# Optimization experiments

Measured on AMD Instinct MI355X. Metric: run time of the kernel, lower is better.

The kernel has to match this reference:

```python
import jax, jax.numpy as jnp
import numpy as np

N_HEAD = 16
N_FEAT = 1024
D_K = N_FEAT // N_HEAD


def setup_inputs() -> dict:
    key = jax.random.key(0)
    ks = jax.random.split(key, 12)
    B, T, F = 4, 2048, N_FEAT
    s = 1.0 / np.sqrt(F)
    return {
        "query": jax.random.normal(ks[0], (B, T, F), dtype=jnp.float32),
        "key": jax.random.normal(ks[1], (B, T, F), dtype=jnp.float32),
        "value": jax.random.normal(ks[2], (B, T, F), dtype=jnp.float32),
        "mask": jnp.ones((B, 1, T), dtype=jnp.int32),
        "Wq": jax.random.normal(ks[3], (F, F), dtype=jnp.float32) * s,
        "bq": jax.random.normal(ks[4], (F,), dtype=jnp.float32) * 0.01,
        "Wk": jax.random.normal(ks[5], (F, F), dtype=jnp.float32) * s,
        "bk": jax.random.normal(ks[6], (F,), dtype=jnp.float32) * 0.01,
        "Wv": jax.random.normal(ks[7], (F, F), dtype=jnp.float32) * s,
        "bv": jax.random.normal(ks[8], (F,), dtype=jnp.float32) * 0.01,
        "Wo": jax.random.normal(ks[9], (F, F), dtype=jnp.float32) * s,
        "bo": jax.random.normal(ks[10], (F,), dtype=jnp.float32) * 0.01,
    }


def reference(query, key, value, mask, Wq, bq, Wk, bk, Wv, bv, Wo, bo):
    B, Tq, F = query.shape
    Tk = key.shape[1]
    h, dk = N_HEAD, D_K
    # torch nn.Linear: y = x @ W.T + b ; then view [B,T,h,dk] and transpose to [B,h,T,dk]
    q = (query @ Wq.T + bq).reshape(B, Tq, h, dk).transpose(0, 2, 1, 3)
    k = (key @ Wk.T + bk).reshape(B, Tk, h, dk).transpose(0, 2, 1, 3)
    v = (value @ Wv.T + bv).reshape(B, Tk, h, dk).transpose(0, 2, 1, 3)
    scale = 1.0 / np.sqrt(dk).astype(np.float32)
    scores = jnp.einsum("bhqd,bhkd->bhqk", q, k) * scale  # [B,h,Tq,Tk]
    # mask [B,1,Tk] -> unsqueeze(1) -> [B,1,1,Tk], True where mask == 0 (padded)
    pad = (mask[:, None, :, :] == 0)
    min_value = jnp.finfo(scores.dtype).min
    scores = jnp.where(pad, min_value, scores)
    atten = jax.nn.softmax(scores, axis=-1)
    atten = jnp.where(pad, 0.0, atten)
    # dropout_rate = 0.0 (eval): identity
    x = jnp.einsum("bhqk,bhkd->bhqd", atten, v)  # [B,h,Tq,dk]
    x = x.transpose(0, 2, 1, 3).reshape(B, Tq, h * dk)
    return x @ Wo.T + bo
```

## Files before the change

### kernel.cpp

```cpp
#include <hip/hip_runtime.h>
#include <hip/hip_bf16.h>


typedef unsigned short u16;
typedef unsigned long long u64;
typedef __attribute__((ext_vector_type(8))) short short8;
typedef __attribute__((ext_vector_type(4))) float f32x4;
typedef __attribute__((ext_vector_type(16))) float f32x16;
typedef __attribute__((ext_vector_type(4))) unsigned int u32x4;

#define GLOAD16(g, l) __builtin_amdgcn_global_load_lds( \
    (const __attribute__((address_space(1))) unsigned int*)(g), \
    (__attribute__((address_space(3))) unsigned int*)(l), 16, 0, 0)

__device__ __forceinline__ u16 f2bf(float x) {
  unsigned int u = __float_as_uint(x);
  return (u16)((u + 0x7fffu + ((u >> 16) & 1u)) >> 16);
}

__device__ __forceinline__ float fexp2(float x) {
#if __has_builtin(__builtin_amdgcn_exp2f)
  return __builtin_amdgcn_exp2f(x);
#else
  return exp2f(x);
#endif
}

__device__ __forceinline__ unsigned cvtpk(float lo, float hi) {
  unsigned r;
  asm("v_cvt_pk_bf16_f32 %0, %1, %2" : "=v"(r) : "v"(lo), "v"(hi));
  return r;
}

struct CvtArgs {
  const float* src[4];
  u16* dst[4];
};

__global__ __launch_bounds__(256) void cvt_multi(CvtArgs a, int shift) {
  const int id = blockIdx.x * 256 + threadIdx.x;
  const int seg = id >> shift;
  const int off = id & ((1 << shift) - 1);
  float4 v = ((const float4*)a.src[seg])[off];
  ushort4 o;
  o.x = f2bf(v.x); o.y = f2bf(v.y); o.z = f2bf(v.z); o.w = f2bf(v.w);
  ((ushort4*)a.dst[seg])[off] = o;
}

template <int EPI, int AF32>
__global__ __launch_bounds__(256) void gemm_bt(const void* __restrict__ Ap,
                                               const u16* __restrict__ Bw,
                                               const float* __restrict__ bias,
                                               void* __restrict__ Cout,
                                               float scale) {
  __shared__ __align__(16) char As[16384];
  __shared__ __align__(16) char Bs[16384];
  const int t = threadIdx.x;
  const int lane = t & 63;
  const int w = t >> 6;
  const int wm = w >> 1, wn = w & 1;
  const int l15 = lane & 15, l4 = lane >> 4;

  const int bid = blockIdx.x;
  const int swz = (bid & 7) * 64 + (bid >> 3);
  const int brow = swz >> 3;
  const int bcol = swz & 7;

  f32x4 acc[4][4] = {};

  const int srow = t >> 3;
  const int sbyte = (t & 7) * 16;
  const int arj = t >> 4;
  const int acol = t & 15;

  for (int kt = 0; kt < 16; ++kt) {
    const int k0 = kt * 64;
    __syncthreads();
    if constexpr (AF32) {
      const float* Ag = (const float*)Ap;
      float4 areg[8];
#pragma unroll
      for (int j = 0; j < 8; ++j)
        areg[j] = *(const float4*)(Ag + (size_t)(brow * 128 + j * 16 + arj) * 1024 +
                                   k0 + acol * 4);
#pragma unroll
      for (int i = 0; i < 4; ++i) {
        const int r = i * 32 + srow;
        const int sb = sbyte ^ ((r & 7) << 4);
        GLOAD16((const char*)(Bw + (size_t)(bcol * 128 + r) * 1024 + k0) + sb,
                Bs + i * 4096 + t * 16);
      }
#pragma unroll
      for (int j = 0; j < 8; ++j) {
        const int r = j * 16 + arj;
        uint2 pk = make_uint2(cvtpk(areg[j].x, areg[j].y), cvtpk(areg[j].z, areg[j].w));
        *(uint2*)(As + r * 128 + ((acol * 8) ^ ((r & 7) << 4))) = pk;
      }
    } else {
      const u16* Ag = (const u16*)Ap;
#pragma unroll
      for (int i = 0; i < 4; ++i) {
        const int r = i * 32 + srow;
        const int sb = sbyte ^ ((r & 7) << 4);
        GLOAD16((const char*)(Ag + (size_t)(brow * 128 + r) * 1024 + k0) + sb,
                As + i * 4096 + t * 16);
        GLOAD16((const char*)(Bw + (size_t)(bcol * 128 + r) * 1024 + k0) + sb,
                Bs + i * 4096 + t * 16);
      }
    }
    __syncthreads();
#pragma unroll
    for (int kf = 0; kf < 2; ++kf) {
      short8 af[4], bfv[4];
#pragma unroll
      for (int mi = 0; mi < 4; ++mi) {
        const int r = wm * 64 + mi * 16 + l15;
        af[mi] = *(const short8*)(As + r * 128 + ((kf * 64 + l4 * 16) ^ ((r & 7) << 4)));
      }
#pragma unroll
      for (int ni = 0; ni < 4; ++ni) {
        const int r = wn * 64 + ni * 16 + l15;
        bfv[ni] = *(const short8*)(Bs + r * 128 + ((kf * 64 + l4 * 16) ^ ((r & 7) << 4)));
      }
#pragma unroll
      for (int mi = 0; mi < 4; ++mi)
#pragma unroll
        for (int ni = 0; ni < 4; ++ni)
          acc[mi][ni] = __builtin_amdgcn_mfma_f32_16x16x32_bf16(
              af[mi], bfv[ni], acc[mi][ni], 0, 0, 0);
    }
  }

#pragma unroll
  for (int ni = 0; ni < 4; ++ni) {
    const int n = bcol * 128 + wn * 64 + ni * 16 + l15;
    const float bn = bias[n];
#pragma unroll
    for (int mi = 0; mi < 4; ++mi) {
      const int mb = brow * 128 + wm * 64 + mi * 16 + l4 * 4;
#pragma unroll
      for (int r = 0; r < 4; ++r) {
        const float v = acc[mi][ni][r] + bn;
        const int m = mb + r;
        const int b_ = m >> 11, tok = m & 2047, h_ = n >> 6, d = n & 63;
        if (EPI == 0) {
          ((u16*)Cout)[(((size_t)(b_ * 16 + h_) * 2048 + tok) << 6) + d] = f2bf(v * scale);
        } else if (EPI == 2) {
          ((u16*)Cout)[(((size_t)(b_ * 16 + h_) * 64 + d) << 11) + tok] = f2bf(v);
        } else {
          ((float*)Cout)[(size_t)m * 1024 + n] = v;
        }
      }
    }
  }
}

__global__ __launch_bounds__(256, 2) void attn_fwd10(const u16* __restrict__ Q,
                                                     const u16* __restrict__ Kp,
                                                     const u16* __restrict__ Vt,
                                                     const int* __restrict__ mask,
                                                     u16* __restrict__ ctx) {
  __shared__ u16 Ks[2][64 * 64];
  __shared__ u16 Vs[2][64 * 64];

  const int t = threadIdx.x, lane = t & 63, w = t >> 6;
  const int q31 = lane & 31, hi = lane >> 5;

  const int bid = blockIdx.x;
  const int swz = (bid & 7) * 64 + (bid >> 3);
  const int bh = swz >> 3;
  const int b_ = bh >> 4, h_ = bh & 15;
  const int q0 = (swz & 7) * 256 + w * 64;
  const size_t headO = (size_t)bh * 131072;

  short8 qfA[4], qfB[4];
  {
    const u16* qrowA = Q + headO + (size_t)(q0 + q31) * 64 + hi * 8;
    const u16* qrowB = qrowA + 32 * 64;
#pragma unroll
    for (int ds = 0; ds < 4; ++ds) {
      qfA[ds] = *(const short8*)(qrowA + ds * 16);
      qfB[ds] = *(const short8*)(qrowB + ds * 16);
    }
  }

  const int srow = t >> 3;
  const int sbyte = (t & 7) * 16;

#define STAGE_KV(bufi, kb)                                                      \
  {                                                                             \
    _Pragma("unroll") for (int i = 0; i < 2; ++i) {                             \
      const int r = i * 32 + srow;                                              \
      const int sb = sbyte ^ ((r & 7) << 4);                                    \
      GLOAD16((const char*)(Kp + headO + (size_t)((kb) + r) * 64) + sb,         \
              &Ks[bufi][(i * 4096 + t * 16) >> 1]);                             \
      GLOAD16((const char*)(Vt + headO + (size_t)r * 2048 + (kb)) + sb,         \
              &Vs[bufi][(i * 4096 + t * 16) >> 1]);                             \
    }                                                                           \
  }

#define SOFTMAX(sA, sB, hh)                                                     \
  {                                                                             \
    if (bits == ~0ull) {                                                        \
      _Pragma("unroll") for (int r = 0; r < 16; ++r) {                          \
        sA[r] = fexp2(sA[r]); sB[r] = fexp2(sB[r]);                             \
      }                                                                         \
    } else {                                                                    \
      _Pragma("unroll") for (int r = 0; r < 16; ++r) {                          \
        const int k0 = (hh) * 32 + (r & 3) + 8 * (r >> 2) + 4 * hi;             \
        const bool on = (bits >> k0) & 1;                                       \
        sA[r] = on ? fexp2(sA[r]) : 0.f;                                        \
        sB[r] = on ? fexp2(sB[r]) : 0.f;                                        \
      }                                                                         \
    }                                                                           \
    float a0 = 0.f, a1 = 0.f, b0 = 0.f, b1 = 0.f;                               \
    _Pragma("unroll") for (int r = 0; r < 16; r += 2) {                         \
      a0 += sA[r]; a1 += sA[r + 1];                                             \
      b0 += sB[r]; b1 += sB[r + 1];                                             \
    }                                                                           \
    lA += a0 + a1;                                                              \
    lB += b0 + b1;                                                              \
  }

#define PACK(sv, pfa, pfb)                                                      \
  {                                                                             \
    const unsigned w0 = cvtpk(sv[0], sv[1]),   w1 = cvtpk(sv[2], sv[3]);        \
    const unsigned w2 = cvtpk(sv[4], sv[5]),   w3 = cvtpk(sv[6], sv[7]);        \
    const unsigned w4 = cvtpk(sv[8], sv[9]),   w5 = cvtpk(sv[10], sv[11]);      \
    const unsigned w6 = cvtpk(sv[12], sv[13]), w7 = cvtpk(sv[14], sv[15]);      \
    const unsigned x0 = (unsigned)__shfl_xor((int)(hi ? w0 : w2), 32);          \
    const unsigned x1 = (unsigned)__shfl_xor((int)(hi ? w1 : w3), 32);          \
    const unsigned y0 = (unsigned)__shfl_xor((int)(hi ? w4 : w6), 32);          \
    const unsigned y1 = (unsigned)__shfl_xor((int)(hi ? w5 : w7), 32);          \
    u32x4 fa = hi ? (u32x4){x0, x1, w2, w3} : (u32x4){w0, w1, x0, x1};          \
    u32x4 fb = hi ? (u32x4){y0, y1, w6, w7} : (u32x4){w4, w5, y0, y1};          \
    pfa = __builtin_bit_cast(short8, fa);                                       \
    pfb = __builtin_bit_cast(short8, fb);                                       \
  }

#define PV(hh, pA0, pA1, pB0, pB1)                                              \
  {                                                                             \
    const int rb0 = q31 * 128, rb1 = (32 + q31) * 128;                          \
    const int c0 = ((hh) * 64 + kcol) ^ rswz;                                   \
    const int c1 = ((hh) * 64 + 32 + kcol) ^ rswz;                              \
    short8 va;                                                                  \
    va = *(const short8*)&Vs[buf][(rb0 + c0) >> 1];                             \
    oA0 = __builtin_amdgcn_mfma_f32_32x32x16_bf16(va, pA0, oA0, 0, 0, 0);       \
    oB0 = __builtin_amdgcn_mfma_f32_32x32x16_bf16(va, pB0, oB0, 0, 0, 0);       \
    va = *(const short8*)&Vs[buf][(rb0 + c1) >> 1];                             \
    oA0 = __builtin_amdgcn_mfma_f32_32x32x16_bf16(va, pA1, oA0, 0, 0, 0);       \
    oB0 = __builtin_amdgcn_mfma_f32_32x32x16_bf16(va, pB1, oB0, 0, 0, 0);       \
    va = *(const short8*)&Vs[buf][(rb1 + c0) >> 1];                             \
    oA1 = __builtin_amdgcn_mfma_f32_32x32x16_bf16(va, pA0, oA1, 0, 0, 0);       \
    oB1 = __builtin_amdgcn_mfma_f32_32x32x16_bf16(va, pB0, oB1, 0, 0, 0);       \
    va = *(const short8*)&Vs[buf][(rb1 + c1) >> 1];                             \
    oA1 = __builtin_amdgcn_mfma_f32_32x32x16_bf16(va, pA1, oA1, 0, 0, 0);       \
    oB1 = __builtin_amdgcn_mfma_f32_32x32x16_bf16(va, pB1, oB1, 0, 0, 0);       \
  }

  f32x16 oA0 = {}, oA1 = {}, oB0 = {}, oB1 = {};
  float lA = 0.f, lB = 0.f;
  const int kcol = hi * 16;
  const int rswz = (q31 & 7) << 4;

  STAGE_KV(0, 0);
  int mk = mask[b_ * 2048 + lane];
  __syncthreads();

  int buf = 0;
  for (int kt = 0; kt < 32; ++kt) {
    const int kb = kt * 64;
    if (kt + 1 < 32) STAGE_KV(buf ^ 1, kb + 64);
    const int mk_next = (kt + 1 < 32) ? mask[b_ * 2048 + kb + 64 + lane] : 0;
    const u64 bits = __ballot(mk != 0);

    f32x16 sA0 = {}, sB0 = {}, sA1 = {}, sB1 = {};
    __builtin_amdgcn_s_setprio(1);
#pragma unroll
    for (int ds = 0; ds < 4; ++ds) {
      const int cb = (ds * 32 + kcol) ^ rswz;
      short8 ka0 = *(const short8*)&Ks[buf][(q31 * 128 + cb) >> 1];
      short8 ka1 = *(const short8*)&Ks[buf][((32 + q31) * 128 + cb) >> 1];
      sA0 = __builtin_amdgcn_mfma_f32_32x32x16_bf16(ka0, qfA[ds], sA0, 0, 0, 0);
      sB0 = __builtin_amdgcn_mfma_f32_32x32x16_bf16(ka0, qfB[ds], sB0, 0, 0, 0);
      sA1 = __builtin_amdgcn_mfma_f32_32x32x16_bf16(ka1, qfA[ds], sA1, 0, 0, 0);
      sB1 = __builtin_amdgcn_mfma_f32_32x32x16_bf16(ka1, qfB[ds], sB1, 0, 0, 0);
    }
    __builtin_amdgcn_s_setprio(0);

    SOFTMAX(sA0, sB0, 0);
    short8 pA0, pA1, pB0, pB1;
    PACK(sA0, pA0, pA1);
    PACK(sB0, pB0, pB1);

    __builtin_amdgcn_s_setprio(1);
    PV(0, pA0, pA1, pB0, pB1);
    __builtin_amdgcn_s_setprio(0);

    SOFTMAX(sA1, sB1, 1);
    PACK(sA1, pA0, pA1);
    PACK(sB1, pB0, pB1);

    __builtin_amdgcn_s_setprio(1);
    PV(1, pA0, pA1, pB0, pB1);
    __builtin_amdgcn_s_setprio(0);

    mk = mk_next;
    __syncthreads();
    buf ^= 1;
  }
#undef STAGE_KV
#undef SOFTMAX
#undef PV

  lA += __shfl_xor(lA, 32);
  lB += __shfl_xor(lB, 32);
  const float invA = lA > 0.f ? 1.f / lA : 0.f;
  const float invB = lB > 0.f ? 1.f / lB : 0.f;
  const int tokA = q0 + q31;
  u16* crowA = ctx + ((size_t)b_ * 2048 + tokA) * 1024 + h_ * 64 + 4 * hi;
  u16* crowB = crowA + 32 * 1024;
#pragma unroll
  for (int g = 0; g < 4; ++g) {
    unsigned u0, u1;
    u0 = cvtpk(oA0[4 * g + 0] * invA, oA0[4 * g + 1] * invA);
    u1 = cvtpk(oA0[4 * g + 2] * invA, oA0[4 * g + 3] * invA);
    *(uint2*)(crowA + 8 * g) = make_uint2(u0, u1);
    u0 = cvtpk(oA1[4 * g + 0] * invA, oA1[4 * g + 1] * invA);
    u1 = cvtpk(oA1[4 * g + 2] * invA, oA1[4 * g + 3] * invA);
    *(uint2*)(crowA + 32 + 8 * g) = make_uint2(u0, u1);
    u0 = cvtpk(oB0[4 * g + 0] * invB, oB0[4 * g + 1] * invB);
    u1 = cvtpk(oB0[4 * g + 2] * invB, oB0[4 * g + 3] * invB);
    *(uint2*)(crowB + 8 * g) = make_uint2(u0, u1);
    u0 = cvtpk(oB1[4 * g + 0] * invB, oB1[4 * g + 1] * invB);
    u1 = cvtpk(oB1[4 * g + 2] * invB, oB1[4 * g + 3] * invB);
    *(uint2*)(crowB + 32 + 8 * g) = make_uint2(u0, u1);
  }
}

extern "C" void kernel_launch(void* const* d_in, const int* in_sizes, int n_in,
                              void* d_out, int out_size, void* d_ws, size_t ws_size,
                              hipStream_t stream) {
  const float* q_in = (const float*)d_in[0];
  const float* k_in = (const float*)d_in[1];
  const float* v_in = (const float*)d_in[2];
  const int*   mask = (const int*)d_in[3];
  const float* Wq = (const float*)d_in[4];
  const float* bq = (const float*)d_in[5];
  const float* Wk = (const float*)d_in[6];
  const float* bk = (const float*)d_in[7];
  const float* Wv = (const float*)d_in[8];
  const float* bv = (const float*)d_in[9];
  const float* Wo = (const float*)d_in[10];
  const float* bo = (const float*)d_in[11];
  float* out = (float*)d_out;

  char* ws = (char*)d_ws;
  u16* ctx = (u16*)(ws);
  u16* Qp = (u16*)(ws + 50331648);
  u16* Kp = (u16*)(ws + 67108864);
  u16* Vtb = (u16*)(ws + 83886080);
  u16* wqb = (u16*)(ws + 100663296);
  u16* wkb = (u16*)(ws + 102760448);
  u16* wvb = (u16*)(ws + 104857600);
  u16* wob = (u16*)(ws + 106954752);

  CvtArgs wts;
  wts.src[0] = Wq;  wts.src[1] = Wk;  wts.src[2] = Wv;  wts.src[3] = Wo;
  wts.dst[0] = wqb; wts.dst[1] = wkb; wts.dst[2] = wvb; wts.dst[3] = wob;
  cvt_multi<<<4 * 1024, 256, 0, stream>>>(wts, 18);

  const float C_SCALE = 0.18033688011112042f;
  gemm_bt<0, 1><<<512, 256, 0, stream>>>(q_in, wqb, bq, Qp, C_SCALE);
  gemm_bt<0, 1><<<512, 256, 0, stream>>>(k_in, wkb, bk, Kp, 1.0f);
  gemm_bt<2, 1><<<512, 256, 0, stream>>>(v_in, wvb, bv, Vtb, 1.0f);

  attn_fwd10<<<512, 256, 0, stream>>>(Qp, Kp, Vtb, mask, ctx);

  gemm_bt<1, 0><<<512, 256, 0, stream>>>(ctx, wob, bo, out, 1.0f);
}
```

Baseline: 221.9 us.

## Double-buffer GEMM LDS tiles to overlap global loads with MFMA

The projection GEMM now uses two LDS buffers per operand and prefetches the next K tile while computing on the current one. This removes one barrier per iteration and hides global-load latency behind MFMA work. It also raises MFMA wave priority with s_setprio around the matrix loop. The cost is doubled LDS use (64KB per block), which may cut occupancy, plus extra live registers for the prefetched fp32 A tile.

```diff
diff --git a/kernel.cpp b/kernel.cpp
--- a/kernel.cpp
+++ b/kernel.cpp
@@ -53,8 +53,8 @@
                                                const float* __restrict__ bias,
                                                void* __restrict__ Cout,
                                                float scale) {
-  __shared__ __align__(16) char As[16384];
-  __shared__ __align__(16) char Bs[16384];
+  __shared__ __align__(16) char As[2][16384];
+  __shared__ __align__(16) char Bs[2][16384];
   const int t = threadIdx.x;
   const int lane = t & 63;
   const int w = t >> 6;
@@ -67,69 +67,91 @@
   const int bcol = swz & 7;
 
   f32x4 acc[4][4] = {};
+  float4 areg[8];
 
   const int srow = t >> 3;
   const int sbyte = (t & 7) * 16;
   const int arj = t >> 4;
   const int acol = t & 15;
 
+#define ALOADR(k0)                                                               \
+  {                                                                              \
+    _Pragma("unroll") for (int j = 0; j < 8; ++j)                                \
+      areg[j] = *(const float4*)((const float*)Ap +                              \
+                 (size_t)(brow * 128 + j * 16 + arj) * 1024 + (k0) + acol * 4);  \
+  }
+#define AWRITE(bufi)                                                             \
+  {                                                                              \
+    _Pragma("unroll") for (int j = 0; j < 8; ++j) {                              \
+      const int r = j * 16 + arj;                                                \
+      uint2 pk = make_uint2(cvtpk(areg[j].x, areg[j].y),                         \
+                            cvtpk(areg[j].z, areg[j].w));                        \
+      *(uint2*)(As[bufi] + r * 128 + ((acol * 8) ^ ((r & 7) << 4))) = pk;        \
+    }                                                                            \
+  }
+#define STAGEA16(bufi, k0)                                                       \
+  {                                                                              \
+    _Pragma("unroll") for (int i = 0; i < 4; ++i) {                              \
+      const int r = i * 32 + srow;                                               \
+      const int sb = sbyte ^ ((r & 7) << 4);                                     \
+      GLOAD16((const char*)((const u16*)Ap + (size_t)(brow * 128 + r) * 1024 +   \
+              (k0)) + sb, As[bufi] + i * 4096 + t * 16);                         \
+    }                                                                            \
+  }
+#define STAGEB(bufi, k0)                                                         \
+  {                                                                              \
+    _Pragma("unroll") for (int i = 0; i < 4; ++i) {                              \
+      const int r = i * 32 + srow;                                               \
+      const int sb = sbyte ^ ((r & 7) << 4);                                     \
+      GLOAD16((const char*)(Bw + (size_t)(bcol * 128 + r) * 1024 + (k0)) + sb,   \
+              Bs[bufi] + i * 4096 + t * 16);                                     \
+    }                                                                            \
+  }
+
+  if constexpr (AF32) { ALOADR(0); } else { STAGEA16(0, 0); }
+  STAGEB(0, 0);
+  if constexpr (AF32) AWRITE(0);
+  __syncthreads();
+
+  int buf = 0;
   for (int kt = 0; kt < 16; ++kt) {
-    const int k0 = kt * 64;
-    __syncthreads();
-    if constexpr (AF32) {
-      const float* Ag = (const float*)Ap;
-      float4 areg[8];
-#pragma unroll
-      for (int j = 0; j < 8; ++j)
-        areg[j] = *(const float4*)(Ag + (size_t)(brow * 128 + j * 16 + arj) * 1024 +
-                                   k0 + acol * 4);
-#pragma unroll
-      for (int i = 0; i < 4; ++i) {
-        const int r = i * 32 + srow;
-        const int sb = sbyte ^ ((r & 7) << 4);
-        GLOAD16((const char*)(Bw + (size_t)(bcol * 128 + r) * 1024 + k0) + sb,
-                Bs + i * 4096 + t * 16);
-      }
-#pragma unroll
-      for (int j = 0; j < 8; ++j) {
-        const int r = j * 16 + arj;
-        uint2 pk = make_uint2(cvtpk(areg[j].x, areg[j].y), cvtpk(areg[j].z, areg[j].w));
-        *(uint2*)(As + r * 128 + ((acol * 8) ^ ((r & 7) << 4))) = pk;
-      }
-    } else {
-      const u16* Ag = (const u16*)Ap;
-#pragma unroll
-      for (int i = 0; i < 4; ++i) {
-        const int r = i * 32 + srow;
-        const int sb = sbyte ^ ((r & 7) << 4);
-        GLOAD16((const char*)(Ag + (size_t)(brow * 128 + r) * 1024 + k0) + sb,
-                As + i * 4096 + t * 16);
-        GLOAD16((const char*)(Bw + (size_t)(bcol * 128 + r) * 1024 + k0) + sb,
-                Bs + i * 4096 + t * 16);
-      }
+    const int kn = kt * 64 + 64;
+    if (kt < 15) {
+      if constexpr (AF32) { ALOADR(kn); } else { STAGEA16(buf ^ 1, kn); }
+      STAGEB(buf ^ 1, kn);
     }
-    __syncthreads();
 #pragma unroll
     for (int kf = 0; kf < 2; ++kf) {
       short8 af[4], bfv[4];
 #pragma unroll
       for (int mi = 0; mi < 4; ++mi) {
         const int r = wm * 64 + mi * 16 + l15;
-        af[mi] = *(const short8*)(As + r * 128 + ((kf * 64 + l4 * 16) ^ ((r & 7) << 4)));
+        af[mi] = *(const short8*)(As[buf] + r * 128 +
+                                  ((kf * 64 + l4 * 16) ^ ((r & 7) << 4)));
       }
 #pragma unroll
       for (int ni = 0; ni < 4; ++ni) {
         const int r = wn * 64 + ni * 16 + l15;
-        bfv[ni] = *(const short8*)(Bs + r * 128 + ((kf * 64 + l4 * 16) ^ ((r & 7) << 4)));
+        bfv[ni] = *(const short8*)(Bs[buf] + r * 128 +
+                                   ((kf * 64 + l4 * 16) ^ ((r & 7) << 4)));
       }
+      __builtin_amdgcn_s_setprio(1);
 #pragma unroll
       for (int mi = 0; mi < 4; ++mi)
 #pragma unroll
         for (int ni = 0; ni < 4; ++ni)
           acc[mi][ni] = __builtin_amdgcn_mfma_f32_16x16x32_bf16(
               af[mi], bfv[ni], acc[mi][ni], 0, 0, 0);
+      __builtin_amdgcn_s_setprio(0);
     }
-  }
+    if (AF32 && kt < 15) AWRITE(buf ^ 1);
+    __syncthreads();
+    buf ^= 1;
+  }
+#undef ALOADR
+#undef AWRITE
+#undef STAGEA16
+#undef STAGEB
 
 #pragma unroll
   for (int ni = 0; ni < 4; ++ni) {
```

Result: no change. 218.4 us (-1.6%).
